# Optimization experiments

Hardware: AMD Instinct MI355X
Metric: run time of the kernel (lower is better)

Reference implementation:

```python
import jax, jax.numpy as jnp
import numpy as np

N_HEAD = 12
N_EMBD = 768

def setup_inputs() -> dict:
    key = jax.random.key(0)
    k1, k2, k3 = jax.random.split(key, 3)
    B, T, C = 4, 2048, N_EMBD
    x = jax.random.normal(k1, (B, T, C), dtype=jnp.float32)
    w_attn = jax.random.normal(k2, (C, 3 * C), dtype=jnp.float32) * (C ** -0.5)
    b_attn = jnp.zeros((3 * C,), dtype=jnp.float32)
    w_proj = jax.random.normal(k3, (C, C), dtype=jnp.float32) * (C ** -0.5)
    b_proj = jnp.zeros((C,), dtype=jnp.float32)
    return {"x": x, "w_attn": w_attn, "b_attn": b_attn, "w_proj": w_proj, "b_proj": b_proj}

def reference(x, w_attn, b_attn, w_proj, b_proj):
    B, T, C = x.shape
    H = N_HEAD
    D = C // H
    qkv = x @ w_attn + b_attn  # [B,T,3C]
    q, k, v = jnp.split(qkv, 3, axis=-1)
    # [B,H,T,D]
    q = q.reshape(B, T, H, D).transpose(0, 2, 1, 3)
    k = k.reshape(B, T, H, D).transpose(0, 2, 1, 3)
    v = v.reshape(B, T, H, D).transpose(0, 2, 1, 3)
    # NOTE: source scales by n_embd**-0.5, not head_dim**-0.5
    scores = jnp.einsum('bhqd,bhkd->bhqk', q, k) * (C ** -0.5)
    causal = jnp.triu(jnp.ones((T, T), dtype=bool), k=1)  # True above diagonal
    scores = jnp.where(causal, -jnp.inf, scores)
    attn = jax.nn.softmax(scores, axis=-1)
    out = jnp.einsum('bhqk,bhkd->bhqd', attn, v)  # [B,H,T,D]
    out = out.transpose(0, 2, 1, 3).reshape(B, T, C)
    return out @ w_proj + b_proj
```

## Files before the change

kernel.cpp:

```cpp
#include <hip/hip_runtime.h>
#include <cstdint>
#include <cstddef>

typedef __attribute__((ext_vector_type(8))) short bf8_t;
typedef __attribute__((ext_vector_type(4))) float f4_t;
typedef __attribute__((ext_vector_type(16))) float f16v_t;
typedef __attribute__((ext_vector_type(2))) unsigned u2_t;
typedef __attribute__((ext_vector_type(4))) unsigned u4_t;

#define DEVFN static __device__ __forceinline__
#define MFMA16(a, b, c) __builtin_amdgcn_mfma_f32_16x16x32_bf16(a, b, c, 0, 0, 0)
#define MFMA32(a, b, c) __builtin_amdgcn_mfma_f32_32x32x16_bf16(a, b, c, 0, 0, 0)

constexpr float kQscale = 0.05205877317700523f;

DEVFN short f2bs(float f) {
  uint32_t u = __builtin_bit_cast(uint32_t, f);
  u = (u + 0x7FFFu + ((u >> 16) & 1u)) >> 16;
  return (short)(uint16_t)u;
}

DEVFN unsigned cvtpk(float lo, float hi) {
  unsigned r;
  asm("v_cvt_pk_bf16_f32 %0, %1, %2" : "=v"(r) : "v"(lo), "v"(hi));
  return r;
}

DEVFN float red2_sum(float v) { return v + __shfl_xor(v, 32, 64); }

DEVFN void gload16(const void* g, void* l) {
  __builtin_amdgcn_global_load_lds(
      (const __attribute__((address_space(1))) void*)g,
      (__attribute__((address_space(3))) void*)l, 16, 0, 0);
}

__global__ __launch_bounds__(256) void cvt_f32_bf16(const float* __restrict__ in,
                                                    short* __restrict__ out) {
  int i = blockIdx.x * 256 + threadIdx.x;
  const f4_t* p = (const f4_t*)in + (size_t)i * 2;
  f4_t a = p[0], b = p[1];
  bf8_t h;
  h[0] = f2bs(a[0]); h[1] = f2bs(a[1]); h[2] = f2bs(a[2]); h[3] = f2bs(a[3]);
  h[4] = f2bs(b[0]); h[5] = f2bs(b[1]); h[6] = f2bs(b[2]); h[7] = f2bs(b[3]);
  *((bf8_t*)out + i) = h;
}

__global__ void transpose_cvt(const float* __restrict__ w, short* __restrict__ wT,
                              int K, int N) {
  __shared__ float tile[32][33];
  int n0 = blockIdx.x << 5, k0 = blockIdx.y << 5;
  int tx = threadIdx.x, ty = threadIdx.y;
#pragma unroll
  for (int i = 0; i < 4; ++i)
    tile[ty * 4 + i][tx] = w[(size_t)(k0 + ty * 4 + i) * N + n0 + tx];
  __syncthreads();
#pragma unroll
  for (int i = 0; i < 4; ++i)
    wT[(size_t)(n0 + ty * 4 + i) * K + k0 + tx] = f2bs(tile[tx][ty * 4 + i]);
}

template <int EPI>
__global__ __launch_bounds__(256) void gemm_bf16(
    const short* __restrict__ A, const short* __restrict__ Bt,
    const float* __restrict__ bias, float* __restrict__ outF,
    short* __restrict__ qb, short* __restrict__ kb, short* __restrict__ vtb,
    int Mdim, int Ndim, int Kdim) {
  __shared__ char smem[65536];
  const int nbx = gridDim.x;
  const int bid = blockIdx.x + nbx * blockIdx.y;
  const int xcd = bid & 7, slot = bid >> 3;
  const int mp = xcd + ((slot / nbx) << 3);
  const int np = slot % nbx;
  const int m0 = mp << 7, n0 = np << 7;
  const int tid = threadIdx.x;
  const int lane = tid & 63, wid = tid >> 6;
  const int wr = wid >> 1, wc = wid & 1;
  const int g = lane >> 4, cl = lane & 15;
  const int ldb = Kdim << 1;

  f4_t acc[4][4];
#pragma unroll
  for (int mi = 0; mi < 4; ++mi)
#pragma unroll
    for (int ni = 0; ni < 4; ++ni) acc[mi][ni] = (f4_t){0.f, 0.f, 0.f, 0.f};

  const char* ga = (const char*)(A + (size_t)m0 * Kdim);
  const char* gb = (const char*)(Bt + (size_t)n0 * Kdim);
  auto stage = [&](int b, int ks) {
    const int k0b = ks << 7;
    char* Ab = smem + (b << 14);
    char* Bb = smem + 32768 + (b << 14);
#pragma unroll
    for (int i = 0; i < 4; ++i) {
      const int doff = (wid << 12) + (i << 10);
      const int boff = doff + lane * 16;
      const int row = boff >> 7;
      const int src = row * ldb + k0b + ((boff & 127) ^ ((row & 7) << 4));
      gload16(ga + src, Ab + doff);
      gload16(gb + src, Bb + doff);
    }
  };

  const int nk = Kdim >> 6;
  stage(0, 0);
  __syncthreads();

  int cur = 0;
  for (int ks = 0; ks < nk; ++ks) {
    const int ksn = (ks + 1 < nk) ? ks + 1 : ks;
    stage(cur ^ 1, ksn);
    const char* Ab = smem + (cur << 14);
    const char* Bb = smem + 32768 + (cur << 14);
#pragma unroll
    for (int kk = 0; kk < 2; ++kk) {
      bf8_t af[4], bfv[4];
#pragma unroll
      for (int mi = 0; mi < 4; ++mi) {
        int lrow = (wr << 6) + (mi << 4) + cl;
        af[mi] = *(const bf8_t*)&Ab[(lrow << 7) + ((((kk << 2) + g) ^ (lrow & 7)) << 4)];
      }
#pragma unroll
      for (int ni = 0; ni < 4; ++ni) {
        int lrow = (wc << 6) + (ni << 4) + cl;
        bfv[ni] = *(const bf8_t*)&Bb[(lrow << 7) + ((((kk << 2) + g) ^ (lrow & 7)) << 4)];
      }
#pragma unroll
      for (int mi = 0; mi < 4; ++mi)
#pragma unroll
        for (int ni = 0; ni < 4; ++ni)
          acc[mi][ni] = MFMA16(af[mi], bfv[ni], acc[mi][ni]);
    }
    __syncthreads();
    cur ^= 1;
  }

  if constexpr (EPI == 1) {
#pragma unroll
    for (int ni = 0; ni < 4; ++ni) {
      const int n = n0 + (wc << 6) + (ni << 4) + cl;
      const float bv = bias[n];
#pragma unroll
      for (int mi = 0; mi < 4; ++mi)
#pragma unroll
        for (int r = 0; r < 4; ++r) {
          const int m = m0 + (wr << 6) + (mi << 4) + (g << 2) + r;
          outF[(size_t)m * 768 + n] = acc[mi][ni][r] + bv;
        }
    }
  } else {
    short* T = (short*)smem;
    const int sec = n0 / 768;
    const float qs = (sec == 0) ? kQscale : 1.0f;
#pragma unroll
    for (int ni = 0; ni < 4; ++ni) {
      const float bv = bias[n0 + (wc << 6) + (ni << 4) + cl];
      const int colT = (wc << 6) + (ni << 4) + cl;
#pragma unroll
      for (int mi = 0; mi < 4; ++mi)
#pragma unroll
        for (int r = 0; r < 4; ++r) {
          const int row = (wr << 6) + (mi << 4) + (g << 2) + r;
          T[row * 132 + colT] = f2bs((acc[mi][ni][r] + bv) * qs);
        }
    }
    __syncthreads();
    if (sec < 2) {
      short* dst0 = (sec == 0) ? qb : kb;
      const int tl = tid & 127, hh2 = tid >> 7;
      const int m = m0 + tl, b = m >> 11, t = m & 2047;
      const int hh = ((n0 - sec * 768) >> 6) + hh2;
      short* dst = dst0 + (size_t)(b * 12 + hh) * 131072 + (size_t)t * 64;
      const short* src = T + tl * 132 + hh2 * 64;
#pragma unroll
      for (int j = 0; j < 8; ++j)
        *(bf8_t*)(dst + j * 8) = *(const bf8_t*)(src + j * 8);
    } else {
      const int chunk = tid & 15;
      const int m = m0 + (chunk << 3);
      const int b = m >> 11, t = m & 2047;
#pragma unroll
      for (int c8 = 0; c8 < 8; ++c8) {
        const int dl = (tid >> 4) + (c8 << 4);
        const int nloc = n0 - 1536 + dl;
        const int hh = nloc >> 6, d = nloc & 63;
        bf8_t tmp;
#pragma unroll
        for (int j = 0; j < 8; ++j)
          tmp[j] = T[((chunk << 3) + j) * 132 + dl];
        *(bf8_t*)(vtb + (size_t)(b * 12 + hh) * 131072 + (size_t)d * 2048 + t) = tmp;
      }
    }
  }
}

__global__ __launch_bounds__(256, 2) void attn_fwd(const short* __restrict__ Q,
                                                   const short* __restrict__ K,
                                                   const short* __restrict__ Vt,
                                                   short* __restrict__ O) {
  __shared__ char kv_lds[2][16384];
  const int tid = threadIdx.x;
  const int lane = tid & 63, wid = tid >> 6;
  const int blk = blockIdx.x;
  const int bh = blk % 48;
  const int qg = 15 - blk / 48;
  const int qt = (qg << 2) + wid;
  const int q0 = qt << 5;
  const int col = lane & 31, hi = lane >> 5;

  const short* Qb = Q + (size_t)bh * 131072;
  const short* Kb = K + (size_t)bh * 131072;
  const short* Vb = Vt + (size_t)bh * 131072;

  bf8_t qf[4];
#pragma unroll
  for (int dc = 0; dc < 4; ++dc)
    qf[dc] = *(const bf8_t*)(Qb + (size_t)(q0 + col) * 64 + dc * 16 + hi * 8);

  const f16v_t zf = {0.f,0.f,0.f,0.f,0.f,0.f,0.f,0.f,0.f,0.f,0.f,0.f,0.f,0.f,0.f,0.f};
  f16v_t o0 = zf, o1 = zf;
  float ls[4] = {0.f, 0.f, 0.f, 0.f};

  const int ns_own = (q0 + 95) >> 6;
  const int ns_max = (qg << 1) + 2;
  const int kxor = (col & 7) << 4;

  auto stage = [&](int b, int kcs) {
    char* buf = &kv_lds[b][0];
    if (wid < 2) {
      const char* g = (const char*)(Kb + (size_t)kcs * 64);
#pragma unroll
      for (int i = 0; i < 4; ++i) {
        const int doff = (wid << 12) + (i << 10);
        const int boff = doff + lane * 16;
        const int src = boff ^ (((boff >> 7) & 7) << 4);
        gload16(g + src, buf + doff);
      }
    } else {
      const char* g = (const char*)Vb + (size_t)kcs * 2;
#pragma unroll
      for (int i = 0; i < 4; ++i) {
        const int doff = ((wid - 2) << 12) + (i << 10);
        const int boff = doff + lane * 16;
        const int row = boff >> 7;
        const int src = row * 4096 + ((boff & 127) ^ ((row & 7) << 4));
        gload16(g + src, buf + 8192 + doff);
      }
    }
  };

  stage(0, 0);
  __syncthreads();

  int cur = 0;
  for (int st = 0; st < ns_max; ++st) {
    int kcn = (st + 1) << 6;
    if (kcn > 1984) kcn = 1984;
    stage(cur ^ 1, kcn);

    if (st < ns_own) {
      const int kc = st << 6;
      const char* Kl = &kv_lds[cur][0];
      const char* Vl = &kv_lds[cur][8192];
      f16v_t s0 = zf, s1 = zf;
#pragma unroll
      for (int dc = 0; dc < 4; ++dc) {
        const int fo = (dc * 32 + hi * 16) ^ kxor;
        bf8_t k0 = *(const bf8_t*)(Kl + col * 128 + fo);
        bf8_t k1 = *(const bf8_t*)(Kl + (32 + col) * 128 + fo);
        __builtin_amdgcn_s_setprio(1);
        s0 = MFMA32(k0, qf[dc], s0);
        s1 = MFMA32(k1, qf[dc], s1);
        __builtin_amdgcn_s_setprio(0);
      }
      if (kc + 63 > q0) {
        const int qq = q0 + col;
#pragma unroll
        for (int r = 0; r < 16; ++r) {
          const int kb_ = kc + (r & 3) + 8 * (r >> 2) + 4 * hi;
          if (kb_ > qq) s0[r] = -1e30f;
          if (kb_ + 32 > qq) s1[r] = -1e30f;
        }
      }
#pragma unroll
      for (int r = 0; r < 16; ++r) {
        s0[r] = __builtin_amdgcn_exp2f(s0[r]);
        s1[r] = __builtin_amdgcn_exp2f(s1[r]);
      }
#pragma unroll
      for (int r = 0; r < 4; ++r)
        ls[r] += ((s0[r] + s0[r + 4]) + (s0[r + 8] + s0[r + 12])) +
                 ((s1[r] + s1[r + 4]) + (s1[r + 8] + s1[r + 12]));
#pragma unroll
      for (int c = 0; c < 4; ++c) {
        const int b8 = (c & 1) * 8;
        float p0, p1, p2, p3, p4, p5, p6, p7;
        if (c < 2) {
          p0 = s0[b8+0]; p1 = s0[b8+1]; p2 = s0[b8+2]; p3 = s0[b8+3];
          p4 = s0[b8+4]; p5 = s0[b8+5]; p6 = s0[b8+6]; p7 = s0[b8+7];
        } else {
          p0 = s1[b8+0]; p1 = s1[b8+1]; p2 = s1[b8+2]; p3 = s1[b8+3];
          p4 = s1[b8+4]; p5 = s1[b8+5]; p6 = s1[b8+6]; p7 = s1[b8+7];
        }
        unsigned w0 = cvtpk(p0, p1), w1 = cvtpk(p2, p3);
        unsigned w2 = cvtpk(p4, p5), w3 = cvtpk(p6, p7);
        unsigned x0 = (unsigned)__shfl_xor((int)w0, 32, 64);
        unsigned x1 = (unsigned)__shfl_xor((int)w1, 32, 64);
        unsigned x2 = (unsigned)__shfl_xor((int)w2, 32, 64);
        unsigned x3 = (unsigned)__shfl_xor((int)w3, 32, 64);
        unsigned T0 = hi ? x2 : w0;
        unsigned T1 = hi ? x3 : w1;
        unsigned T2 = hi ? w2 : x0;
        unsigned T3 = hi ? w3 : x1;
        const bf8_t pf = __builtin_bit_cast(bf8_t, (u4_t){T0, T1, T2, T3});
        const int vo = (c * 32 + hi * 16) ^ kxor;
        bf8_t v0 = *(const bf8_t*)(Vl + col * 128 + vo);
        bf8_t v1 = *(const bf8_t*)(Vl + (32 + col) * 128 + vo);
        __builtin_amdgcn_s_setprio(1);
        o0 = MFMA32(v0, pf, o0);
        o1 = MFMA32(v1, pf, o1);
        __builtin_amdgcn_s_setprio(0);
      }
    }
    __syncthreads();
    cur ^= 1;
  }

  const float l = red2_sum((ls[0] + ls[1]) + (ls[2] + ls[3]));
  const float rl = 1.0f / l;
  const int b_ = bh / 12, hh = bh % 12;
  short* Op = O + (size_t)b_ * 2048 * 768 + (size_t)(q0 + col) * 768 + hh * 64;
#pragma unroll
  for (int rq = 0; rq < 4; ++rq) {
    u2_t w0, w1;
    w0[0] = cvtpk(o0[4*rq+0] * rl, o0[4*rq+1] * rl);
    w0[1] = cvtpk(o0[4*rq+2] * rl, o0[4*rq+3] * rl);
    w1[0] = cvtpk(o1[4*rq+0] * rl, o1[4*rq+1] * rl);
    w1[1] = cvtpk(o1[4*rq+2] * rl, o1[4*rq+3] * rl);
    *(u2_t*)(Op + rq * 8 + hi * 4) = w0;
    *(u2_t*)(Op + 32 + rq * 8 + hi * 4) = w1;
  }
}

extern "C" void kernel_launch(void* const* d_in, const int* in_sizes, int n_in,
                              void* d_out, int out_size, void* d_ws, size_t ws_size,
                              hipStream_t stream) {
  const float* x      = (const float*)d_in[0];
  const float* w_attn = (const float*)d_in[1];
  const float* b_attn = (const float*)d_in[2];
  const float* w_proj = (const float*)d_in[3];
  const float* b_proj = (const float*)d_in[4];
  float* out = (float*)d_out;

  const size_t QSZ = (size_t)4 * 12 * 2048 * 64;
  short* ws  = (short*)d_ws;
  short* qb  = ws;
  short* kb  = qb + QSZ;
  short* vtb = kb + QSZ;
  short* xb  = vtb + QSZ;
  short* ob  = xb;
  short* wat = xb + QSZ;
  short* wpt = wat + (size_t)2304 * 768;

  cvt_f32_bf16<<<3072, 256, 0, stream>>>(x, xb);
  transpose_cvt<<<dim3(72, 24), dim3(32, 8), 0, stream>>>(w_attn, wat, 768, 2304);
  transpose_cvt<<<dim3(24, 24), dim3(32, 8), 0, stream>>>(w_proj, wpt, 768, 768);

  gemm_bf16<0><<<dim3(18, 64), 256, 0, stream>>>(xb, wat, b_attn, nullptr,
                                                 qb, kb, vtb, 8192, 2304, 768);
  attn_fwd<<<768, 256, 0, stream>>>(qb, kb, vtb, ob);
  gemm_bf16<1><<<dim3(6, 64), 256, 0, stream>>>(ob, wpt, b_proj, out,
                                                nullptr, nullptr, nullptr, 8192, 768, 768);
}
```

Baseline: 136.9 us.

## Merge prep kernels into one launch and stage 128-key tiles in attention

After: 132.1 us. 1.04x faster.

```diff
diff --git a/kernel.cpp b/kernel.cpp
--- a/kernel.cpp
+++ b/kernel.cpp
@@ -34,29 +34,44 @@
       (__attribute__((address_space(3))) void*)l, 16, 0, 0);
 }
 
-__global__ __launch_bounds__(256) void cvt_f32_bf16(const float* __restrict__ in,
-                                                    short* __restrict__ out) {
-  int i = blockIdx.x * 256 + threadIdx.x;
-  const f4_t* p = (const f4_t*)in + (size_t)i * 2;
-  f4_t a = p[0], b = p[1];
-  bf8_t h;
-  h[0] = f2bs(a[0]); h[1] = f2bs(a[1]); h[2] = f2bs(a[2]); h[3] = f2bs(a[3]);
-  h[4] = f2bs(b[0]); h[5] = f2bs(b[1]); h[6] = f2bs(b[2]); h[7] = f2bs(b[3]);
-  *((bf8_t*)out + i) = h;
-}
-
-__global__ void transpose_cvt(const float* __restrict__ w, short* __restrict__ wT,
-                              int K, int N) {
+__global__ __launch_bounds__(256) void prep(const float* __restrict__ x,
+                                            short* __restrict__ xb,
+                                            const float* __restrict__ w_attn,
+                                            short* __restrict__ wat,
+                                            const float* __restrict__ w_proj,
+                                            short* __restrict__ wpt) {
   __shared__ float tile[32][33];
-  int n0 = blockIdx.x << 5, k0 = blockIdx.y << 5;
-  int tx = threadIdx.x, ty = threadIdx.y;
+  const int blk = blockIdx.x, tid = threadIdx.x;
+  if (blk < 3072) {
+    const int i = blk * 256 + tid;
+    const f4_t* p = (const f4_t*)x + (size_t)i * 2;
+    f4_t a = p[0], b = p[1];
+    bf8_t h;
+    h[0] = f2bs(a[0]); h[1] = f2bs(a[1]); h[2] = f2bs(a[2]); h[3] = f2bs(a[3]);
+    h[4] = f2bs(b[0]); h[5] = f2bs(b[1]); h[6] = f2bs(b[2]); h[7] = f2bs(b[3]);
+    *((bf8_t*)xb + i) = h;
+    return;
+  }
+  const float* w;
+  short* wT;
+  int N, n0, k0;
+  if (blk < 4800) {
+    const int bb = blk - 3072;
+    w = w_attn; wT = wat; N = 2304;
+    n0 = (bb % 72) << 5; k0 = (bb / 72) << 5;
+  } else {
+    const int bb = blk - 4800;
+    w = w_proj; wT = wpt; N = 768;
+    n0 = (bb % 24) << 5; k0 = (bb / 24) << 5;
+  }
+  const int tx = tid & 31, ty = tid >> 5;
 #pragma unroll
   for (int i = 0; i < 4; ++i)
     tile[ty * 4 + i][tx] = w[(size_t)(k0 + ty * 4 + i) * N + n0 + tx];
   __syncthreads();
 #pragma unroll
   for (int i = 0; i < 4; ++i)
-    wT[(size_t)(n0 + ty * 4 + i) * K + k0 + tx] = f2bs(tile[tx][ty * 4 + i]);
+    wT[(size_t)(n0 + ty * 4 + i) * 768 + k0 + tx] = f2bs(tile[tx][ty * 4 + i]);
 }
 
 template <int EPI>
@@ -197,7 +212,7 @@
                                                    const short* __restrict__ K,
                                                    const short* __restrict__ Vt,
                                                    short* __restrict__ O) {
-  __shared__ char kv_lds[2][16384];
+  __shared__ char kv_lds[2][32768];
   const int tid = threadIdx.x;
   const int lane = tid & 63, wid = tid >> 6;
   const int blk = blockIdx.x;
@@ -220,8 +235,7 @@
   f16v_t o0 = zf, o1 = zf;
   float ls[4] = {0.f, 0.f, 0.f, 0.f};
 
-  const int ns_own = (q0 + 95) >> 6;
-  const int ns_max = (qg << 1) + 2;
+  const int nt = qg + 1;
   const int kxor = (col & 7) << 4;
 
   auto stage = [&](int b, int kcs) {
@@ -229,8 +243,8 @@
     if (wid < 2) {
       const char* g = (const char*)(Kb + (size_t)kcs * 64);
 #pragma unroll
-      for (int i = 0; i < 4; ++i) {
-        const int doff = (wid << 12) + (i << 10);
+      for (int i = 0; i < 8; ++i) {
+        const int doff = (wid << 13) + (i << 10);
         const int boff = doff + lane * 16;
         const int src = boff ^ (((boff >> 7) & 7) << 4);
         gload16(g + src, buf + doff);
@@ -238,12 +252,12 @@
     } else {
       const char* g = (const char*)Vb + (size_t)kcs * 2;
 #pragma unroll
-      for (int i = 0; i < 4; ++i) {
-        const int doff = ((wid - 2) << 12) + (i << 10);
+      for (int i = 0; i < 8; ++i) {
+        const int doff = ((wid - 2) << 13) + (i << 10);
         const int boff = doff + lane * 16;
-        const int row = boff >> 7;
-        const int src = row * 4096 + ((boff & 127) ^ ((row & 7) << 4));
-        gload16(g + src, buf + 8192 + doff);
+        const int row = boff >> 8;
+        const int src = row * 4096 + ((boff & 255) ^ ((row & 7) << 4));
+        gload16(g + src, buf + 16384 + doff);
       }
     }
   };
@@ -252,73 +266,76 @@
   __syncthreads();
 
   int cur = 0;
-  for (int st = 0; st < ns_max; ++st) {
-    int kcn = (st + 1) << 6;
-    if (kcn > 1984) kcn = 1984;
+  for (int st = 0; st < nt; ++st) {
+    int kcn = (st + 1) << 7;
+    if (kcn > 1920) kcn = 1920;
     stage(cur ^ 1, kcn);
 
-    if (st < ns_own) {
-      const int kc = st << 6;
-      const char* Kl = &kv_lds[cur][0];
-      const char* Vl = &kv_lds[cur][8192];
-      f16v_t s0 = zf, s1 = zf;
-#pragma unroll
-      for (int dc = 0; dc < 4; ++dc) {
-        const int fo = (dc * 32 + hi * 16) ^ kxor;
-        bf8_t k0 = *(const bf8_t*)(Kl + col * 128 + fo);
-        bf8_t k1 = *(const bf8_t*)(Kl + (32 + col) * 128 + fo);
-        __builtin_amdgcn_s_setprio(1);
-        s0 = MFMA32(k0, qf[dc], s0);
-        s1 = MFMA32(k1, qf[dc], s1);
-        __builtin_amdgcn_s_setprio(0);
-      }
-      if (kc + 63 > q0) {
-        const int qq = q0 + col;
+#pragma unroll
+    for (int h = 0; h < 2; ++h) {
+      const int kc = (st << 7) + (h << 6);
+      if (kc < q0 + 32) {
+        const char* Kl = &kv_lds[cur][h << 13];
+        const char* Vl = &kv_lds[cur][16384];
+        f16v_t s0 = zf, s1 = zf;
+#pragma unroll
+        for (int dc = 0; dc < 4; ++dc) {
+          const int fo = (dc * 32 + hi * 16) ^ kxor;
+          bf8_t k0 = *(const bf8_t*)(Kl + col * 128 + fo);
+          bf8_t k1 = *(const bf8_t*)(Kl + (32 + col) * 128 + fo);
+          __builtin_amdgcn_s_setprio(1);
+          s0 = MFMA32(k0, qf[dc], s0);
+          s1 = MFMA32(k1, qf[dc], s1);
+          __builtin_amdgcn_s_setprio(0);
+        }
+        if (kc + 63 > q0) {
+          const int qq = q0 + col;
+#pragma unroll
+          for (int r = 0; r < 16; ++r) {
+            const int kb_ = kc + (r & 3) + 8 * (r >> 2) + 4 * hi;
+            if (kb_ > qq) s0[r] = -1e30f;
+            if (kb_ + 32 > qq) s1[r] = -1e30f;
+          }
+        }
 #pragma unroll
         for (int r = 0; r < 16; ++r) {
-          const int kb_ = kc + (r & 3) + 8 * (r >> 2) + 4 * hi;
-          if (kb_ > qq) s0[r] = -1e30f;
-          if (kb_ + 32 > qq) s1[r] = -1e30f;
-        }
-      }
-#pragma unroll
-      for (int r = 0; r < 16; ++r) {
-        s0[r] = __builtin_amdgcn_exp2f(s0[r]);
-        s1[r] = __builtin_amdgcn_exp2f(s1[r]);
-      }
-#pragma unroll
-      for (int r = 0; r < 4; ++r)
-        ls[r] += ((s0[r] + s0[r + 4]) + (s0[r + 8] + s0[r + 12])) +
-                 ((s1[r] + s1[r + 4]) + (s1[r + 8] + s1[r + 12]));
-#pragma unroll
-      for (int c = 0; c < 4; ++c) {
-        const int b8 = (c & 1) * 8;
-        float p0, p1, p2, p3, p4, p5, p6, p7;
-        if (c < 2) {
-          p0 = s0[b8+0]; p1 = s0[b8+1]; p2 = s0[b8+2]; p3 = s0[b8+3];
-          p4 = s0[b8+4]; p5 = s0[b8+5]; p6 = s0[b8+6]; p7 = s0[b8+7];
-        } else {
-          p0 = s1[b8+0]; p1 = s1[b8+1]; p2 = s1[b8+2]; p3 = s1[b8+3];
-          p4 = s1[b8+4]; p5 = s1[b8+5]; p6 = s1[b8+6]; p7 = s1[b8+7];
-        }
-        unsigned w0 = cvtpk(p0, p1), w1 = cvtpk(p2, p3);
-        unsigned w2 = cvtpk(p4, p5), w3 = cvtpk(p6, p7);
-        unsigned x0 = (unsigned)__shfl_xor((int)w0, 32, 64);
-        unsigned x1 = (unsigned)__shfl_xor((int)w1, 32, 64);
-        unsigned x2 = (unsigned)__shfl_xor((int)w2, 32, 64);
-        unsigned x3 = (unsigned)__shfl_xor((int)w3, 32, 64);
-        unsigned T0 = hi ? x2 : w0;
-        unsigned T1 = hi ? x3 : w1;
-        unsigned T2 = hi ? w2 : x0;
-        unsigned T3 = hi ? w3 : x1;
-        const bf8_t pf = __builtin_bit_cast(bf8_t, (u4_t){T0, T1, T2, T3});
-        const int vo = (c * 32 + hi * 16) ^ kxor;
-        bf8_t v0 = *(const bf8_t*)(Vl + col * 128 + vo);
-        bf8_t v1 = *(const bf8_t*)(Vl + (32 + col) * 128 + vo);
-        __builtin_amdgcn_s_setprio(1);
-        o0 = MFMA32(v0, pf, o0);
-        o1 = MFMA32(v1, pf, o1);
-        __builtin_amdgcn_s_setprio(0);
+          s0[r] = __builtin_amdgcn_exp2f(s0[r]);
+          s1[r] = __builtin_amdgcn_exp2f(s1[r]);
+        }
+#pragma unroll
+        for (int r = 0; r < 4; ++r)
+          ls[r] += ((s0[r] + s0[r + 4]) + (s0[r + 8] + s0[r + 12])) +
+                   ((s1[r] + s1[r + 4]) + (s1[r + 8] + s1[r + 12]));
+#pragma unroll
+        for (int c = 0; c < 4; ++c) {
+          const int b8 = (c & 1) * 8;
+          float p0, p1, p2, p3, p4, p5, p6, p7;
+          if (c < 2) {
+            p0 = s0[b8+0]; p1 = s0[b8+1]; p2 = s0[b8+2]; p3 = s0[b8+3];
+            p4 = s0[b8+4]; p5 = s0[b8+5]; p6 = s0[b8+6]; p7 = s0[b8+7];
+          } else {
+            p0 = s1[b8+0]; p1 = s1[b8+1]; p2 = s1[b8+2]; p3 = s1[b8+3];
+            p4 = s1[b8+4]; p5 = s1[b8+5]; p6 = s1[b8+6]; p7 = s1[b8+7];
+          }
+          unsigned w0 = cvtpk(p0, p1), w1 = cvtpk(p2, p3);
+          unsigned w2 = cvtpk(p4, p5), w3 = cvtpk(p6, p7);
+          unsigned x0 = (unsigned)__shfl_xor((int)w0, 32, 64);
+          unsigned x1 = (unsigned)__shfl_xor((int)w1, 32, 64);
+          unsigned x2 = (unsigned)__shfl_xor((int)w2, 32, 64);
+          unsigned x3 = (unsigned)__shfl_xor((int)w3, 32, 64);
+          unsigned T0 = hi ? x2 : w0;
+          unsigned T1 = hi ? x3 : w1;
+          unsigned T2 = hi ? w2 : x0;
+          unsigned T3 = hi ? w3 : x1;
+          const bf8_t pf = __builtin_bit_cast(bf8_t, (u4_t){T0, T1, T2, T3});
+          const int vo = ((h << 7) + c * 32 + hi * 16) ^ kxor;
+          bf8_t v0 = *(const bf8_t*)(Vl + col * 256 + vo);
+          bf8_t v1 = *(const bf8_t*)(Vl + (32 + col) * 256 + vo);
+          __builtin_amdgcn_s_setprio(1);
+          o0 = MFMA32(v0, pf, o0);
+          o1 = MFMA32(v1, pf, o1);
+          __builtin_amdgcn_s_setprio(0);
+        }
       }
     }
     __syncthreads();
@@ -361,9 +378,7 @@
   short* wat = xb + QSZ;
   short* wpt = wat + (size_t)2304 * 768;
 
-  cvt_f32_bf16<<<3072, 256, 0, stream>>>(x, xb);
-  transpose_cvt<<<dim3(72, 24), dim3(32, 8), 0, stream>>>(w_attn, wat, 768, 2304);
-  transpose_cvt<<<dim3(24, 24), dim3(32, 8), 0, stream>>>(w_proj, wpt, 768, 768);
+  prep<<<5376, 256, 0, stream>>>(x, xb, w_attn, wat, w_proj, wpt);
 
   gemm_bf16<0><<<dim3(18, 64), 256, 0, stream>>>(xb, wat, b_attn, nullptr,
                                                  qb, kb, vtb, 8192, 2304, 768);
```
